# Kernel tuning notes

Hardware: AMD Instinct MI355X
Metric: run time of the kernel (lower is better)

Reference implementation:

```python
import jax, jax.numpy as jnp
import numpy as np

SIZE = 100
NUM_PARAMS = 5
DEPTH = 10            # complete binary tree: 2**DEPTH - 1 = 1023 nodes, 512 leaves
NUM_TREES = 1024
NUM_NODES = 2 ** DEPTH - 1


def setup_inputs() -> dict:
    key = jax.random.key(0)
    ks = jax.random.split(key, 7)
    times = jax.random.uniform(ks[0], (NUM_TREES, NUM_NODES), dtype=jnp.float32) + 0.1
    # Linear(1, size): weight column vector + bias
    Qw = jax.random.normal(ks[1], (SIZE,), dtype=jnp.float32) * 0.5
    Qb = jax.random.normal(ks[2], (SIZE,), dtype=jnp.float32) * 0.1
    # Linear(size, size): scaled so deep relu chain stays stable
    Ww = jax.random.normal(ks[3], (SIZE, SIZE), dtype=jnp.float32) * (0.5 / np.sqrt(SIZE))
    Wb = jax.random.normal(ks[4], (SIZE,), dtype=jnp.float32) * 0.1
    # Linear(size, num_params)
    Pw = jax.random.normal(ks[5], (NUM_PARAMS, SIZE), dtype=jnp.float32) * (1.0 / np.sqrt(SIZE))
    Pb = jax.random.normal(ks[6], (NUM_PARAMS,), dtype=jnp.float32) * 0.1
    return {"times": times, "Qw": Qw, "Qb": Qb, "Ww": Ww, "Wb": Wb, "Pw": Pw, "Pb": Pb}


def reference(times, Qw, Qb, Ww, Wb, Pw, Pb):
    """Batched, level-synchronous version of gRNN.traverse over complete binary trees.

    times: [B, 2**D - 1] node times in heap order (node i -> children 2i+1, 2i+2).
    Leaf:     h = relu(Q(t))
    Internal: h = relu(W(h_left + h_right) + Q(t))
    Root output projected to num_params. Same math as the recursive torch code.
    """
    B, N = times.shape
    D = int(np.log2(N + 1))
    # leaf level (deepest): Q(t) = t * Qw + Qb  (Linear(1, size))
    s = 2 ** (D - 1) - 1
    h = jax.nn.relu(times[:, s:s + 2 ** (D - 1), None] * Qw + Qb)  # [B, 2^(D-1), size]
    for d in range(D - 2, -1, -1):  # fixed small loop over tree depth
        s = 2 ** d - 1
        t = times[:, s:s + 2 ** d, None]                 # [B, 2^d, 1]
        comb = h[:, 0::2] + h[:, 1::2]                   # left + right children
        h = jax.nn.relu(jnp.einsum('bns,os->bno', comb, Ww) + Wb + t * Qw + Qb)
    root = h[:, 0]                                       # [B, size]
    return root @ Pw.T + Pb                              # [B, num_params]
```

## Files before the change

kernel.cpp:

```cpp
#include <hip/hip_runtime.h>

typedef _Float16 h8 __attribute__((ext_vector_type(8)));
typedef _Float16 h4 __attribute__((ext_vector_type(4)));
typedef _Float16 h2 __attribute__((ext_vector_type(2)));
typedef float f4 __attribute__((ext_vector_type(4)));

#define NT 7
#define KC 4
#define HSTRIDE 104

__global__ __launch_bounds__(64, 1)
void grnn_fused(const float* __restrict__ times,
                const float* __restrict__ Qw,
                const float* __restrict__ Qb,
                const float* __restrict__ Ww,
                const float* __restrict__ Wb,
                const float* __restrict__ Pw,
                const float* __restrict__ Pb,
                float* __restrict__ out)
{
  __shared__ __align__(16) _Float16 Cs[128][HSTRIDE];
  __shared__ __align__(16) _Float16 trash[512];
  __shared__ __align__(4)  _Float16 ts_fold[512];
  __shared__ __align__(4)  h2 tsp[256];

  const int lane = threadIdx.x;
  const int l15  = lane & 15;
  const int kg   = lane >> 4;
  const int tree = blockIdx.x;

  {
    const float* tg = times + tree * 1023;
    #pragma unroll
    for (int q = 0; q < 4; ++q) {
      const int pr = lane + 64 * q;
      *(h2*)&ts_fold[2 * pr] = (h2){(_Float16)tg[2 * pr], (_Float16)tg[2 * pr + 1]};
      tsp[pr] = (h2){(_Float16)tg[511 + 2 * pr], (_Float16)tg[512 + 2 * pr]};
    }
  }

  h8 wf[NT][KC];
  #pragma unroll
  for (int nt = 0; nt < NT; ++nt) {
    const int r = nt * 16 + l15;
    #pragma unroll
    for (int kc = 0; kc < KC; ++kc) {
      h8 v;
      #pragma unroll
      for (int j = 0; j < 8; ++j) v[j] = (_Float16)0.f;
      if (r < 100) {
        const int kb = kc * 32 + kg * 8;
        if (kc < 3) {
          const f4 w0 = *(const f4*)&Ww[r * 100 + kb];
          const f4 w1 = *(const f4*)&Ww[r * 100 + kb + 4];
          #pragma unroll
          for (int j = 0; j < 4; ++j) {
            v[j]     = (_Float16)w0[j];
            v[j + 4] = (_Float16)w1[j];
          }
        } else if (kg == 0) {
          const f4 w0 = *(const f4*)&Ww[r * 100 + 96];
          #pragma unroll
          for (int j = 0; j < 4; ++j) v[j] = (_Float16)w0[j];
          v[4] = (_Float16)Qw[r];
          v[5] = (_Float16)(Qb[r] + Wb[r]);
        }
      }
      wf[nt][kc] = v;
    }
  }

  h8 qwp[KC], qbp[KC];
  #pragma unroll
  for (int kc = 0; kc < KC; ++kc) {
    const int kb = kc * 32 + kg * 8;
    #pragma unroll
    for (int j = 0; j < 8; ++j) {
      const int ix = kb + j;
      qwp[kc][j] = (ix < 100) ? (_Float16)Qw[ix] : (_Float16)0.f;
      qbp[kc][j] = (ix < 100) ? (_Float16)Qb[ix] : (_Float16)0.f;
    }
  }

#define DO_MT(AFR, MT) do {                                                   \
    const int rw_ = (MT) * 8 + (l15 >> 1);                                    \
    _Float16* pv_ = (l15 & 1) ? &trash[lane * 4] : &Cs[rw_][kg * 4];          \
    _Float16* p6_ = kg ? &trash[lane * 4] : pv_;                              \
    _Pragma("unroll")                                                         \
    for (int nt_ = 0; nt_ < NT; ++nt_) {                                      \
      f4 acc_ = {0.f, 0.f, 0.f, 0.f};                                         \
      _Pragma("unroll")                                                       \
      for (int kc_ = 0; kc_ < KC; ++kc_)                                      \
        acc_ = __builtin_amdgcn_mfma_f32_16x16x32_f16(wf[nt_][kc_],           \
                                                      AFR[kc_], acc_, 0,0,0); \
      h2 c0_ = {(_Float16)acc_[0], (_Float16)acc_[1]};                        \
      h2 c1_ = {(_Float16)acc_[2], (_Float16)acc_[3]};                        \
      const h2 z2_ = {(_Float16)0.f, (_Float16)0.f};                          \
      c0_ = __builtin_elementwise_max(c0_, z2_);                              \
      c1_ = __builtin_elementwise_max(c1_, z2_);                              \
      int d0_ = __builtin_amdgcn_mov_dpp(__builtin_bit_cast(int, c0_),        \
                                         0xB1, 0xF, 0xF, true);               \
      int d1_ = __builtin_amdgcn_mov_dpp(__builtin_bit_cast(int, c1_),        \
                                         0xB1, 0xF, 0xF, true);               \
      c0_ = c0_ + __builtin_bit_cast(h2, d0_);                                \
      c1_ = c1_ + __builtin_bit_cast(h2, d1_);                                \
      h4 hv_ = {c0_[0], c0_[1], c1_[0], c1_[1]};                              \
      *(h4*)((nt_ == 6 ? p6_ : pv_) + nt_ * 16) = hv_;                        \
    }                                                                         \
  } while (0)

#define DO_MT_ROOT(AFR) do {                                                  \
    _Float16* pv_ = (l15 == 0) ? &Cs[0][kg * 4] : &trash[lane * 4];           \
    _Float16* p6_ = kg ? &trash[lane * 4] : pv_;                              \
    _Pragma("unroll")                                                         \
    for (int nt_ = 0; nt_ < NT; ++nt_) {                                      \
      f4 acc_ = {0.f, 0.f, 0.f, 0.f};                                         \
      _Pragma("unroll")                                                       \
      for (int kc_ = 0; kc_ < KC; ++kc_)                                      \
        acc_ = __builtin_amdgcn_mfma_f32_16x16x32_f16(wf[nt_][kc_],           \
                                                      AFR[kc_], acc_, 0,0,0); \
      h2 c0_ = {(_Float16)acc_[0], (_Float16)acc_[1]};                        \
      h2 c1_ = {(_Float16)acc_[2], (_Float16)acc_[3]};                        \
      const h2 z2_ = {(_Float16)0.f, (_Float16)0.f};                          \
      c0_ = __builtin_elementwise_max(c0_, z2_);                              \
      c1_ = __builtin_elementwise_max(c1_, z2_);                              \
      h4 hv_ = {c0_[0], c0_[1], c1_[0], c1_[1]};                              \
      *(h4*)((nt_ == 6 ? p6_ : pv_) + nt_ * 16) = hv_;                        \
    }                                                                         \
  } while (0)

#define LOAD_AFR(AFR, MT, S) do {                                             \
    const int row_ = (MT) * 16 + l15;                                         \
    AFR[0] = *(const h8*)&Cs[row_][kg * 8];                                   \
    AFR[1] = *(const h8*)&Cs[row_][32 + kg * 8];                              \
    AFR[2] = *(const h8*)&Cs[row_][64 + kg * 8];                              \
    h4 lo_ = *(const h4*)&Cs[row_][96];                                       \
    h4 hi_ = {ts_fold[(S) + (MT) * 16 + l15], (_Float16)1.f,                  \
              (_Float16)0.f, (_Float16)0.f};                                  \
    AFR[3] = __builtin_shufflevector(lo_, hi_, 0, 1, 2, 3, 4, 5, 6, 7);       \
  } while (0)

  const h8 z8 = {(_Float16)0.f, (_Float16)0.f, (_Float16)0.f, (_Float16)0.f,
                 (_Float16)0.f, (_Float16)0.f, (_Float16)0.f, (_Float16)0.f};
  #pragma unroll 2
  for (int i = 0; i < 16; ++i) {
    const int m = i * 16 + l15;
    const h2 tp = tsp[m];
    const _Float16 t0 = tp[0], t1 = tp[1];
    h8 afl[KC];
    #pragma unroll
    for (int kc = 0; kc < KC; ++kc) {
      h8 a = qwp[kc] * t0 + qbp[kc];
      h8 b = qwp[kc] * t1 + qbp[kc];
      a = __builtin_elementwise_max(a, z8);
      b = __builtin_elementwise_max(b, z8);
      afl[kc] = a + b;
    }
    afl[3][4] = ts_fold[255 + m];
    afl[3][5] = (_Float16)1.f;
    DO_MT(afl, i);
  }

  h8 af[KC], afn[KC];
  LOAD_AFR(af, 0, 127);
  #pragma unroll 1
  for (int j = 0; j < 14; ++j) {
    const int i = j - ((j < 8) ? 0 : (j < 12) ? 8 : 12);
    if (j < 13) {
      const int j2 = j + 1;
      const int d2 = (j2 < 8) ? 7 : (j2 < 12) ? 6 : 5;
      const int i2 = j2 - ((j2 < 8) ? 0 : (j2 < 12) ? 8 : 12);
      LOAD_AFR(afn, i2, (1 << d2) - 1);
    }
    DO_MT(af, i);
    if (j == 13) LOAD_AFR(afn, 0, 15);
    #pragma unroll
    for (int c = 0; c < KC; ++c) af[c] = afn[c];
  }

  #pragma unroll 1
  for (int d = 4; d >= 1; --d) {
    DO_MT(af, 0);
    LOAD_AFR(afn, 0, (1 << (d - 1)) - 1);
    #pragma unroll
    for (int c = 0; c < KC; ++c) af[c] = afn[c];
  }

  DO_MT_ROOT(af);

  #pragma unroll 1
  for (int p = 0; p < 5; ++p) {
    float v = (float)Cs[0][lane] * Pw[p * 100 + lane];
    if (lane < 36) v += (float)Cs[0][64 + lane] * Pw[p * 100 + 64 + lane];
    v += __shfl_xor(v, 32, 64);
    v += __shfl_xor(v, 16, 64);
    v += __shfl_xor(v, 8, 64);
    v += __shfl_xor(v, 4, 64);
    v += __shfl_xor(v, 2, 64);
    v += __shfl_xor(v, 1, 64);
    if (lane == 0) out[tree * 5 + p] = v + Pb[p];
  }
#undef DO_MT
#undef DO_MT_ROOT
#undef LOAD_AFR
}

extern "C" void kernel_launch(void* const* d_in, const int* in_sizes, int n_in,
                              void* d_out, int out_size, void* d_ws, size_t ws_size,
                              hipStream_t stream) {
  (void)n_in; (void)out_size; (void)d_ws; (void)ws_size;
  const float* times = (const float*)d_in[0];
  const float* Qw = (const float*)d_in[1];
  const float* Qb = (const float*)d_in[2];
  const float* Ww = (const float*)d_in[3];
  const float* Wb = (const float*)d_in[4];
  const float* Pw = (const float*)d_in[5];
  const float* Pb = (const float*)d_in[6];
  float* outp = (float*)d_out;
  const int B = in_sizes[0] / 1023;
  grnn_fused<<<dim3(B), dim3(64), 0, stream>>>(times, Qw, Qb, Ww, Wb, Pw, Pb, outp);
}
```

Baseline: 94.05 us.

## Split each tree across two waves, each owning a half-subtree

Launches 128 threads per tree instead of 64. Each wave independently processes half of the tree's lower levels (leaves through depth 4) on its own subtree rows. After a block barrier, wave 0 finishes the top levels and the output projection. Per-leaf time values are preloaded into registers and the leaf loop is fully unrolled. This roughly halves the serial MFMA chain per tree, at the cost of each wave loading its own copy of the weight fragments, a synchronization point, and an idle second wave during the top levels.

```diff
diff --git a/kernel.cpp b/kernel.cpp
--- a/kernel.cpp
+++ b/kernel.cpp
@@ -9,7 +9,7 @@
 #define KC 4
 #define HSTRIDE 104
 
-__global__ __launch_bounds__(64, 1)
+__global__ __launch_bounds__(128, 1)
 void grnn_fused(const float* __restrict__ times,
                 const float* __restrict__ Qw,
                 const float* __restrict__ Qb,
@@ -24,20 +24,13 @@
   __shared__ __align__(4)  _Float16 ts_fold[512];
   __shared__ __align__(4)  h2 tsp[256];
 
-  const int lane = threadIdx.x;
+  const int tid  = threadIdx.x;
+  const int wave = tid >> 6;
+  const int lane = tid & 63;
   const int l15  = lane & 15;
   const int kg   = lane >> 4;
   const int tree = blockIdx.x;
-
-  {
-    const float* tg = times + tree * 1023;
-    #pragma unroll
-    for (int q = 0; q < 4; ++q) {
-      const int pr = lane + 64 * q;
-      *(h2*)&ts_fold[2 * pr] = (h2){(_Float16)tg[2 * pr], (_Float16)tg[2 * pr + 1]};
-      tsp[pr] = (h2){(_Float16)tg[511 + 2 * pr], (_Float16)tg[512 + 2 * pr]};
-    }
-  }
+  const int PB   = wave << 6;
 
   h8 wf[NT][KC];
   #pragma unroll
@@ -82,8 +75,23 @@
     }
   }
 
-#define DO_MT(AFR, MT) do {                                                   \
-    const int rw_ = (MT) * 8 + (l15 >> 1);                                    \
+  {
+    const float* tg = times + tree * 1023;
+    #pragma unroll
+    for (int q = 0; q < 4; ++q) {
+      const int ix = tid + 128 * q;
+      if (ix < 511) ts_fold[ix] = (_Float16)tg[ix];
+    }
+    #pragma unroll
+    for (int q = 0; q < 2; ++q) {
+      const int pr = tid + 128 * q;
+      tsp[pr] = (h2){(_Float16)tg[511 + 2 * pr], (_Float16)tg[512 + 2 * pr]};
+    }
+  }
+  __syncthreads();
+
+#define DO_MT(AFR, RW) do {                                                   \
+    const int rw_ = (RW);                                                     \
     _Float16* pv_ = (l15 & 1) ? &trash[lane * 4] : &Cs[rw_][kg * 4];          \
     _Float16* p6_ = kg ? &trash[lane * 4] : pv_;                              \
     _Pragma("unroll")                                                         \
@@ -129,24 +137,27 @@
     }                                                                         \
   } while (0)
 
-#define LOAD_AFR(AFR, MT, S) do {                                             \
-    const int row_ = (MT) * 16 + l15;                                         \
+#define LOAD_AFR(AFR, ROW, TSI) do {                                          \
+    const int row_ = (ROW);                                                   \
     AFR[0] = *(const h8*)&Cs[row_][kg * 8];                                   \
     AFR[1] = *(const h8*)&Cs[row_][32 + kg * 8];                              \
     AFR[2] = *(const h8*)&Cs[row_][64 + kg * 8];                              \
     h4 lo_ = *(const h4*)&Cs[row_][96];                                       \
-    h4 hi_ = {ts_fold[(S) + (MT) * 16 + l15], (_Float16)1.f,                  \
-              (_Float16)0.f, (_Float16)0.f};                                  \
+    h4 hi_ = {ts_fold[TSI], (_Float16)1.f, (_Float16)0.f, (_Float16)0.f};     \
     AFR[3] = __builtin_shufflevector(lo_, hi_, 0, 1, 2, 3, 4, 5, 6, 7);       \
   } while (0)
 
+  h2 tpv[8]; _Float16 tfv[8];
+  #pragma unroll
+  for (int i = 0; i < 8; ++i) {
+    tpv[i] = tsp[128 * wave + 16 * i + l15];
+    tfv[i] = ts_fold[255 + 128 * wave + 16 * i + l15];
+  }
   const h8 z8 = {(_Float16)0.f, (_Float16)0.f, (_Float16)0.f, (_Float16)0.f,
                  (_Float16)0.f, (_Float16)0.f, (_Float16)0.f, (_Float16)0.f};
-  #pragma unroll 2
-  for (int i = 0; i < 16; ++i) {
-    const int m = i * 16 + l15;
-    const h2 tp = tsp[m];
-    const _Float16 t0 = tp[0], t1 = tp[1];
+  #pragma unroll
+  for (int i = 0; i < 8; ++i) {
+    const _Float16 t0 = tpv[i][0], t1 = tpv[i][1];
     h8 afl[KC];
     #pragma unroll
     for (int kc = 0; kc < KC; ++kc) {
@@ -156,49 +167,65 @@
       b = __builtin_elementwise_max(b, z8);
       afl[kc] = a + b;
     }
-    afl[3][4] = ts_fold[255 + m];
+    afl[3][4] = tfv[i];
     afl[3][5] = (_Float16)1.f;
-    DO_MT(afl, i);
-  }
-
-  h8 af[KC], afn[KC];
-  LOAD_AFR(af, 0, 127);
-  #pragma unroll 1
-  for (int j = 0; j < 14; ++j) {
-    const int i = j - ((j < 8) ? 0 : (j < 12) ? 8 : 12);
-    if (j < 13) {
-      const int j2 = j + 1;
-      const int d2 = (j2 < 8) ? 7 : (j2 < 12) ? 6 : 5;
-      const int i2 = j2 - ((j2 < 8) ? 0 : (j2 < 12) ? 8 : 12);
-      LOAD_AFR(afn, i2, (1 << d2) - 1);
-    }
-    DO_MT(af, i);
-    if (j == 13) LOAD_AFR(afn, 0, 15);
-    #pragma unroll
-    for (int c = 0; c < KC; ++c) af[c] = afn[c];
-  }
-
-  #pragma unroll 1
-  for (int d = 4; d >= 1; --d) {
-    DO_MT(af, 0);
-    LOAD_AFR(afn, 0, (1 << (d - 1)) - 1);
-    #pragma unroll
-    for (int c = 0; c < KC; ++c) af[c] = afn[c];
-  }
-
-  DO_MT_ROOT(af);
-
-  #pragma unroll 1
-  for (int p = 0; p < 5; ++p) {
-    float v = (float)Cs[0][lane] * Pw[p * 100 + lane];
-    if (lane < 36) v += (float)Cs[0][64 + lane] * Pw[p * 100 + 64 + lane];
-    v += __shfl_xor(v, 32, 64);
-    v += __shfl_xor(v, 16, 64);
-    v += __shfl_xor(v, 8, 64);
-    v += __shfl_xor(v, 4, 64);
-    v += __shfl_xor(v, 2, 64);
-    v += __shfl_xor(v, 1, 64);
-    if (lane == 0) out[tree * 5 + p] = v + Pb[p];
+    DO_MT(afl, PB + 8 * i + (l15 >> 1));
+  }
+
+  {
+    h8 af[KC], afn[KC];
+    LOAD_AFR(af, PB + l15, 127 + 64 * wave + l15);
+    LOAD_AFR(afn, PB + 16 + l15, 127 + 64 * wave + 16 + l15);
+    DO_MT(af, PB + (l15 >> 1));
+    #pragma unroll
+    for (int c = 0; c < KC; ++c) af[c] = afn[c];
+    LOAD_AFR(afn, PB + 32 + l15, 127 + 64 * wave + 32 + l15);
+    DO_MT(af, PB + 16 + (l15 >> 1));
+    #pragma unroll
+    for (int c = 0; c < KC; ++c) af[c] = afn[c];
+    LOAD_AFR(afn, PB + 48 + l15, 127 + 64 * wave + 48 + l15);
+    DO_MT(af, PB + 32 + (l15 >> 1));
+    #pragma unroll
+    for (int c = 0; c < KC; ++c) af[c] = afn[c];
+    LOAD_AFR(afn, PB + 16 * (l15 >> 3) + (l15 & 7), 63 + 32 * wave + l15);
+    DO_MT(af, PB + 48 + (l15 >> 1));
+    #pragma unroll
+    for (int c = 0; c < KC; ++c) af[c] = afn[c];
+    LOAD_AFR(afn, PB + 32 + 16 * (l15 >> 3) + (l15 & 7),
+             63 + 32 * wave + 16 + l15);
+    DO_MT(af, PB + (l15 >> 1));
+    #pragma unroll
+    for (int c = 0; c < KC; ++c) af[c] = afn[c];
+    DO_MT(af, PB + 32 + (l15 >> 1));
+    LOAD_AFR(af, PB + 32 * (l15 >> 3) + (l15 & 7), 31 + 16 * wave + l15);
+    DO_MT(af, PB + (l15 >> 1));
+  }
+  __syncthreads();
+
+  if (wave == 0) {
+    h8 af[KC];
+    LOAD_AFR(af, (l15 < 8) ? l15 : (56 + l15), 15 + l15);
+    DO_MT(af, (l15 >> 1));
+    #pragma unroll 1
+    for (int d = 3; d >= 1; --d) {
+      LOAD_AFR(af, l15, (1 << d) - 1 + l15);
+      DO_MT(af, (l15 >> 1));
+    }
+    LOAD_AFR(af, l15, l15);
+    DO_MT_ROOT(af);
+
+    #pragma unroll 1
+    for (int p = 0; p < 5; ++p) {
+      float v = (float)Cs[0][lane] * Pw[p * 100 + lane];
+      if (lane < 36) v += (float)Cs[0][64 + lane] * Pw[p * 100 + 64 + lane];
+      v += __shfl_xor(v, 32, 64);
+      v += __shfl_xor(v, 16, 64);
+      v += __shfl_xor(v, 8, 64);
+      v += __shfl_xor(v, 4, 64);
+      v += __shfl_xor(v, 2, 64);
+      v += __shfl_xor(v, 1, 64);
+      if (lane == 0) out[tree * 5 + p] = v + Pb[p];
+    }
   }
 #undef DO_MT
 #undef DO_MT_ROOT
@@ -218,5 +245,5 @@
   const float* Pb = (const float*)d_in[6];
   float* outp = (float*)d_out;
   const int B = in_sizes[0] / 1023;
-  grnn_fused<<<dim3(B), dim3(64), 0, stream>>>(times, Qw, Qb, Ww, Wb, Pw, Pb, outp);
+  grnn_fused<<<dim3(B), dim3(128), 0, stream>>>(times, Qw, Qb, Ww, Wb, Pw, Pb, outp);
 }
```

New measurement: 98.56 us. +4.8%, slower.

## Switch tree recurrence to 32x32x16 MFMA tiles with four interleaved accumulators

Applied to the files above, without the earlier changes.

Replaces the 16x16x32 MFMA scheme (7 output tiles x 4 K-chunks, serially dependent per tile) with 32x32x16 MFMAs over 4 feature tiles x 7 K-chunks. Each 32-node batch now runs four independent accumulator chains, which is meant to hide MFMA latency and halve the number of tile passes per level. The change also moves Qw/Qb into shared memory instead of registers and rewrites the epilogue to convert with cvt_pkrtz. In exchange the small upper levels waste more of each larger tile, and the 16-wide accumulators raise register pressure.

```diff
diff --git a/kernel.cpp b/kernel.cpp
--- a/kernel.cpp
+++ b/kernel.cpp
@@ -4,9 +4,8 @@
 typedef _Float16 h4 __attribute__((ext_vector_type(4)));
 typedef _Float16 h2 __attribute__((ext_vector_type(2)));
 typedef float f4 __attribute__((ext_vector_type(4)));
-
-#define NT 7
-#define KC 4
+typedef float f16v __attribute__((ext_vector_type(16)));
+
 #define HSTRIDE 104
 
 __global__ __launch_bounds__(64, 1)
@@ -23,34 +22,48 @@
   __shared__ __align__(16) _Float16 trash[512];
   __shared__ __align__(4)  _Float16 ts_fold[512];
   __shared__ __align__(4)  h2 tsp[256];
+  __shared__ __align__(16) _Float16 qwh[112];
+  __shared__ __align__(16) _Float16 qbh[112];
 
   const int lane = threadIdx.x;
-  const int l15  = lane & 15;
-  const int kg   = lane >> 4;
+  const int c    = lane & 31;
+  const int hw   = lane >> 5;
   const int tree = blockIdx.x;
 
   {
     const float* tg = times + tree * 1023;
     #pragma unroll
+    for (int q = 0; q < 8; ++q) {
+      const int ix = lane + 64 * q;
+      if (ix < 511) ts_fold[ix] = (_Float16)tg[ix];
+    }
+    #pragma unroll
     for (int q = 0; q < 4; ++q) {
       const int pr = lane + 64 * q;
-      *(h2*)&ts_fold[2 * pr] = (h2){(_Float16)tg[2 * pr], (_Float16)tg[2 * pr + 1]};
       tsp[pr] = (h2){(_Float16)tg[511 + 2 * pr], (_Float16)tg[512 + 2 * pr]};
     }
-  }
-
-  h8 wf[NT][KC];
+    #pragma unroll
+    for (int q = 0; q < 2; ++q) {
+      const int ix = lane + 64 * q;
+      if (ix < 112) {
+        qwh[ix] = (ix < 100) ? (_Float16)Qw[ix] : (_Float16)0.f;
+        qbh[ix] = (ix < 100) ? (_Float16)Qb[ix] : (_Float16)0.f;
+      }
+    }
+  }
+
+  h8 wf[4][7];
   #pragma unroll
-  for (int nt = 0; nt < NT; ++nt) {
-    const int r = nt * 16 + l15;
-    #pragma unroll
-    for (int kc = 0; kc < KC; ++kc) {
+  for (int ft = 0; ft < 4; ++ft) {
+    const int r = 32 * ft + c;
+    #pragma unroll
+    for (int kc = 0; kc < 7; ++kc) {
       h8 v;
       #pragma unroll
       for (int j = 0; j < 8; ++j) v[j] = (_Float16)0.f;
       if (r < 100) {
-        const int kb = kc * 32 + kg * 8;
-        if (kc < 3) {
+        if (kc < 6) {
+          const int kb = 16 * kc + 8 * hw;
           const f4 w0 = *(const f4*)&Ww[r * 100 + kb];
           const f4 w1 = *(const f4*)&Ww[r * 100 + kb + 4];
           #pragma unroll
@@ -58,7 +71,7 @@
             v[j]     = (_Float16)w0[j];
             v[j + 4] = (_Float16)w1[j];
           }
-        } else if (kg == 0) {
+        } else if (hw == 0) {
           const f4 w0 = *(const f4*)&Ww[r * 100 + 96];
           #pragma unroll
           for (int j = 0; j < 4; ++j) v[j] = (_Float16)w0[j];
@@ -66,127 +79,131 @@
           v[5] = (_Float16)(Qb[r] + Wb[r]);
         }
       }
-      wf[nt][kc] = v;
-    }
-  }
-
-  h8 qwp[KC], qbp[KC];
-  #pragma unroll
-  for (int kc = 0; kc < KC; ++kc) {
-    const int kb = kc * 32 + kg * 8;
-    #pragma unroll
-    for (int j = 0; j < 8; ++j) {
-      const int ix = kb + j;
-      qwp[kc][j] = (ix < 100) ? (_Float16)Qw[ix] : (_Float16)0.f;
-      qbp[kc][j] = (ix < 100) ? (_Float16)Qb[ix] : (_Float16)0.f;
-    }
-  }
-
-#define DO_MT(AFR, MT) do {                                                   \
-    const int rw_ = (MT) * 8 + (l15 >> 1);                                    \
-    _Float16* pv_ = (l15 & 1) ? &trash[lane * 4] : &Cs[rw_][kg * 4];          \
-    _Float16* p6_ = kg ? &trash[lane * 4] : pv_;                              \
-    _Pragma("unroll")                                                         \
-    for (int nt_ = 0; nt_ < NT; ++nt_) {                                      \
-      f4 acc_ = {0.f, 0.f, 0.f, 0.f};                                         \
-      _Pragma("unroll")                                                       \
-      for (int kc_ = 0; kc_ < KC; ++kc_)                                      \
-        acc_ = __builtin_amdgcn_mfma_f32_16x16x32_f16(wf[nt_][kc_],           \
-                                                      AFR[kc_], acc_, 0,0,0); \
-      h2 c0_ = {(_Float16)acc_[0], (_Float16)acc_[1]};                        \
-      h2 c1_ = {(_Float16)acc_[2], (_Float16)acc_[3]};                        \
-      const h2 z2_ = {(_Float16)0.f, (_Float16)0.f};                          \
-      c0_ = __builtin_elementwise_max(c0_, z2_);                              \
-      c1_ = __builtin_elementwise_max(c1_, z2_);                              \
-      int d0_ = __builtin_amdgcn_mov_dpp(__builtin_bit_cast(int, c0_),        \
-                                         0xB1, 0xF, 0xF, true);               \
-      int d1_ = __builtin_amdgcn_mov_dpp(__builtin_bit_cast(int, c1_),        \
-                                         0xB1, 0xF, 0xF, true);               \
-      c0_ = c0_ + __builtin_bit_cast(h2, d0_);                                \
-      c1_ = c1_ + __builtin_bit_cast(h2, d1_);                                \
-      h4 hv_ = {c0_[0], c0_[1], c1_[0], c1_[1]};                              \
-      *(h4*)((nt_ == 6 ? p6_ : pv_) + nt_ * 16) = hv_;                        \
+      wf[ft][kc] = v;
+    }
+  }
+
+#define DO_TILE(BF, BSE, DODPP) do {                                          \
+    f16v acc_[4];                                                             \
+    _Pragma("unroll")                                                         \
+    for (int ft_ = 0; ft_ < 4; ++ft_)                                         \
+      _Pragma("unroll")                                                       \
+      for (int e_ = 0; e_ < 16; ++e_) acc_[ft_][e_] = 0.f;                    \
+    _Pragma("unroll")                                                         \
+    for (int kc_ = 0; kc_ < 7; ++kc_) {                                       \
+      _Pragma("unroll")                                                       \
+      for (int ft_ = 0; ft_ < 4; ++ft_)                                       \
+        acc_[ft_] = __builtin_amdgcn_mfma_f32_32x32x16_f16(wf[ft_][kc_],      \
+                                              BF[kc_], acc_[ft_], 0, 0, 0);   \
+    }                                                                         \
+    _Float16* b3_ = (hw == 0) ? (BSE) : &trash[lane * 4];                     \
+    _Pragma("unroll")                                                         \
+    for (int ft_ = 0; ft_ < 4; ++ft_) {                                       \
+      _Pragma("unroll")                                                       \
+      for (int g_ = 0; g_ < 4; ++g_) {                                        \
+        if (ft_ < 3 || (g_ == 0)) {                                           \
+          float a0_ = fmaxf(acc_[ft_][4 * g_ + 0], 0.f);                      \
+          float a1_ = fmaxf(acc_[ft_][4 * g_ + 1], 0.f);                      \
+          float a2_ = fmaxf(acc_[ft_][4 * g_ + 2], 0.f);                      \
+          float a3_ = fmaxf(acc_[ft_][4 * g_ + 3], 0.f);                      \
+          h2 lo_ = __builtin_bit_cast(h2,                                     \
+                       __builtin_amdgcn_cvt_pkrtz(a0_, a1_));                 \
+          h2 hi_ = __builtin_bit_cast(h2,                                     \
+                       __builtin_amdgcn_cvt_pkrtz(a2_, a3_));                 \
+          if (DODPP) {                                                        \
+            int d0_ = __builtin_amdgcn_mov_dpp(__builtin_bit_cast(int, lo_),  \
+                                               0xB1, 0xF, 0xF, true);         \
+            int d1_ = __builtin_amdgcn_mov_dpp(__builtin_bit_cast(int, hi_),  \
+                                               0xB1, 0xF, 0xF, true);         \
+            lo_ = lo_ + __builtin_bit_cast(h2, d0_);                          \
+            hi_ = hi_ + __builtin_bit_cast(h2, d1_);                          \
+          }                                                                   \
+          h4 hv_ = {lo_[0], lo_[1], hi_[0], hi_[1]};                          \
+          *(h4*)(((ft_ == 3) ? b3_ : (BSE)) + 32 * ft_ + 8 * g_ + 4 * hw)     \
+              = hv_;                                                          \
+        }                                                                     \
+      }                                                                       \
     }                                                                         \
   } while (0)
 
-#define DO_MT_ROOT(AFR) do {                                                  \
-    _Float16* pv_ = (l15 == 0) ? &Cs[0][kg * 4] : &trash[lane * 4];           \
-    _Float16* p6_ = kg ? &trash[lane * 4] : pv_;                              \
-    _Pragma("unroll")                                                         \
-    for (int nt_ = 0; nt_ < NT; ++nt_) {                                      \
-      f4 acc_ = {0.f, 0.f, 0.f, 0.f};                                         \
-      _Pragma("unroll")                                                       \
-      for (int kc_ = 0; kc_ < KC; ++kc_)                                      \
-        acc_ = __builtin_amdgcn_mfma_f32_16x16x32_f16(wf[nt_][kc_],           \
-                                                      AFR[kc_], acc_, 0,0,0); \
-      h2 c0_ = {(_Float16)acc_[0], (_Float16)acc_[1]};                        \
-      h2 c1_ = {(_Float16)acc_[2], (_Float16)acc_[3]};                        \
-      const h2 z2_ = {(_Float16)0.f, (_Float16)0.f};                          \
-      c0_ = __builtin_elementwise_max(c0_, z2_);                              \
-      c1_ = __builtin_elementwise_max(c1_, z2_);                              \
-      h4 hv_ = {c0_[0], c0_[1], c1_[0], c1_[1]};                              \
-      *(h4*)((nt_ == 6 ? p6_ : pv_) + nt_ * 16) = hv_;                        \
+#define LOAD_B(BF, RBASE, RMASK, TSIB) do {                                   \
+    const int cm_ = c & (RMASK);                                              \
+    const int row_ = (RBASE) + cm_;                                           \
+    _Pragma("unroll")                                                         \
+    for (int kc_ = 0; kc_ < 6; ++kc_)                                         \
+      BF[kc_] = *(const h8*)&Cs[row_][16 * kc_ + 8 * hw];                     \
+    if (hw == 0) {                                                            \
+      h4 lo_ = *(const h4*)&Cs[row_][96];                                     \
+      h4 hi_ = {ts_fold[(TSIB) + cm_], (_Float16)1.f,                         \
+                (_Float16)0.f, (_Float16)0.f};                                \
+      BF[6] = __builtin_shufflevector(lo_, hi_, 0, 1, 2, 3, 4, 5, 6, 7);      \
+    } else {                                                                  \
+      _Pragma("unroll")                                                       \
+      for (int j_ = 0; j_ < 8; ++j_) BF[6][j_] = (_Float16)0.f;               \
     }                                                                         \
   } while (0)
 
-#define LOAD_AFR(AFR, MT, S) do {                                             \
-    const int row_ = (MT) * 16 + l15;                                         \
-    AFR[0] = *(const h8*)&Cs[row_][kg * 8];                                   \
-    AFR[1] = *(const h8*)&Cs[row_][32 + kg * 8];                              \
-    AFR[2] = *(const h8*)&Cs[row_][64 + kg * 8];                              \
-    h4 lo_ = *(const h4*)&Cs[row_][96];                                       \
-    h4 hi_ = {ts_fold[(S) + (MT) * 16 + l15], (_Float16)1.f,                  \
-              (_Float16)0.f, (_Float16)0.f};                                  \
-    AFR[3] = __builtin_shufflevector(lo_, hi_, 0, 1, 2, 3, 4, 5, 6, 7);       \
-  } while (0)
-
-  const h8 z8 = {(_Float16)0.f, (_Float16)0.f, (_Float16)0.f, (_Float16)0.f,
-                 (_Float16)0.f, (_Float16)0.f, (_Float16)0.f, (_Float16)0.f};
+#define BASE_PTR(WROW, NN)                                                    \
+    ((((c & 1) == 0) && (c < (NN))) ? &Cs[(WROW) + (c >> 1)][0]               \
+                                    : &trash[lane * 4])
+
   #pragma unroll 2
-  for (int i = 0; i < 16; ++i) {
-    const int m = i * 16 + l15;
-    const h2 tp = tsp[m];
+  for (int i = 0; i < 8; ++i) {
+    const h2 tp = tsp[32 * i + c];
     const _Float16 t0 = tp[0], t1 = tp[1];
-    h8 afl[KC];
-    #pragma unroll
-    for (int kc = 0; kc < KC; ++kc) {
-      h8 a = qwp[kc] * t0 + qbp[kc];
-      h8 b = qwp[kc] * t1 + qbp[kc];
-      a = __builtin_elementwise_max(a, z8);
-      b = __builtin_elementwise_max(b, z8);
-      afl[kc] = a + b;
-    }
-    afl[3][4] = ts_fold[255 + m];
-    afl[3][5] = (_Float16)1.f;
-    DO_MT(afl, i);
-  }
-
-  h8 af[KC], afn[KC];
-  LOAD_AFR(af, 0, 127);
-  #pragma unroll 1
-  for (int j = 0; j < 14; ++j) {
-    const int i = j - ((j < 8) ? 0 : (j < 12) ? 8 : 12);
-    if (j < 13) {
-      const int j2 = j + 1;
-      const int d2 = (j2 < 8) ? 7 : (j2 < 12) ? 6 : 5;
-      const int i2 = j2 - ((j2 < 8) ? 0 : (j2 < 12) ? 8 : 12);
-      LOAD_AFR(afn, i2, (1 << d2) - 1);
-    }
-    DO_MT(af, i);
-    if (j == 13) LOAD_AFR(afn, 0, 15);
-    #pragma unroll
-    for (int c = 0; c < KC; ++c) af[c] = afn[c];
-  }
-
+    const h8 z8 = {(_Float16)0.f, (_Float16)0.f, (_Float16)0.f, (_Float16)0.f,
+                   (_Float16)0.f, (_Float16)0.f, (_Float16)0.f, (_Float16)0.f};
+    h8 bf[7];
+    #pragma unroll
+    for (int kc = 0; kc < 7; ++kc) {
+      const h8 qw8 = *(const h8*)&qwh[16 * kc + 8 * hw];
+      const h8 qb8 = *(const h8*)&qbh[16 * kc + 8 * hw];
+      h8 a = __builtin_elementwise_max(qw8 * t0 + qb8, z8);
+      h8 b = __builtin_elementwise_max(qw8 * t1 + qb8, z8);
+      bf[kc] = a + b;
+    }
+    if (hw == 0) {
+      bf[6][4] = ts_fold[255 + 32 * i + c];
+      bf[6][5] = (_Float16)1.f;
+    }
+    _Float16* bse = BASE_PTR(16 * i, 32);
+    DO_TILE(bf, bse, 1);
+  }
+
+  #pragma unroll 1
+  for (int i = 0; i < 4; ++i) {
+    h8 bf[7];
+    LOAD_B(bf, 32 * i, 31, 127 + 32 * i);
+    _Float16* bse = BASE_PTR(16 * i, 32);
+    DO_TILE(bf, bse, 1);
+  }
+  #pragma unroll 1
+  for (int i = 0; i < 2; ++i) {
+    h8 bf[7];
+    LOAD_B(bf, 32 * i, 31, 63 + 32 * i);
+    _Float16* bse = BASE_PTR(16 * i, 32);
+    DO_TILE(bf, bse, 1);
+  }
+  {
+    h8 bf[7];
+    LOAD_B(bf, 0, 31, 31);
+    _Float16* bse = BASE_PTR(0, 32);
+    DO_TILE(bf, bse, 1);
+  }
   #pragma unroll 1
   for (int d = 4; d >= 1; --d) {
-    DO_MT(af, 0);
-    LOAD_AFR(afn, 0, (1 << (d - 1)) - 1);
-    #pragma unroll
-    for (int c = 0; c < KC; ++c) af[c] = afn[c];
-  }
-
-  DO_MT_ROOT(af);
+    const int nn = 1 << d;
+    h8 bf[7];
+    LOAD_B(bf, 0, nn - 1, nn - 1);
+    _Float16* bse = BASE_PTR(0, nn);
+    DO_TILE(bf, bse, 1);
+  }
+  {
+    h8 bf[7];
+    LOAD_B(bf, 0, 0, 0);
+    _Float16* bse = (c == 0) ? &Cs[0][0] : &trash[lane * 4];
+    DO_TILE(bf, bse, 0);
+  }
 
   #pragma unroll 1
   for (int p = 0; p < 5; ++p) {
@@ -200,9 +217,9 @@
     v += __shfl_xor(v, 1, 64);
     if (lane == 0) out[tree * 5 + p] = v + Pb[p];
   }
-#undef DO_MT
-#undef DO_MT_ROOT
-#undef LOAD_AFR
+#undef DO_TILE
+#undef LOAD_B
+#undef BASE_PTR
 }
 
 extern "C" void kernel_launch(void* const* d_in, const int* in_sizes, int n_in,
```

Result: slower. 98.17 us (+4.4%).
